# Kernel tuning notes

Measured on AMD Instinct MI355X. Metric: run time of the kernel, lower is better.

The kernel has to match this reference:

```python
import jax, jax.numpy as jnp
import numpy as np

D_MODEL = 256
D_INNER = 512   # expand_factor * d_model
D_STATE = 64
DT_RANK = 4     # ceil(d_model / 64)
D_CONV = 4
B = 8
L = 144


def setup_inputs() -> dict:
    key = jax.random.key(0)
    ks = jax.random.split(key, 8)
    s = lambda k, shp, sc=0.02: jax.random.normal(k, shp, jnp.float32) * sc
    x = jax.random.normal(ks[0], (B, L, D_MODEL), jnp.float32)
    lastin = jnp.zeros((B, D_INNER, D_STATE), jnp.float32)  # accepted but unused by the scan
    W_in = s(ks[1], (2 * D_INNER, D_MODEL))              # in_proj (no bias)
    conv_w = s(ks[2], (D_INNER, 1, D_CONV), 0.1)          # depthwise conv kernel [O, I/groups, K]
    conv_b = jnp.zeros((D_INNER,), jnp.float32)
    W_x = s(ks[3], (DT_RANK + 2 * D_STATE, D_INNER))      # x_proj (no bias)
    W_dt = s(ks[4], (D_INNER, DT_RANK), 0.1)
    b_dt = jnp.full((D_INNER,), -4.0, jnp.float32)        # softplus -> small dt, like mamba init
    A_log = jnp.log(jnp.tile(jnp.arange(1, D_STATE + 1, dtype=jnp.float32), (D_INNER, 1)))
    Dp = jnp.ones((D_INNER,), jnp.float32)
    W_out = s(ks[5], (D_MODEL, D_INNER))                  # out_proj (no bias)
    return dict(x=x, lastin=lastin, W_in=W_in, conv_w=conv_w, conv_b=conv_b,
                W_x=W_x, W_dt=W_dt, b_dt=b_dt, A_log=A_log, Dp=Dp, W_out=W_out)


def _forward(x, lastin, W_in, conv_w, conv_b, W_x, W_dt, b_dt, A_log, Dp, W_out):
    # in_proj and split
    xz = jnp.einsum('bld,ed->ble', x, W_in)               # [B, L, 2*d_inner]
    ix, z = jnp.split(xz, 2, axis=-1)

    # depthwise causal-ish conv1d: torch padding=2 then slice [:L] == padding (2, 1)
    ix = jnp.swapaxes(ix, 1, 2)                            # [B, d_inner, L]
    ix = jax.lax.conv_general_dilated(
        ix, conv_w, window_strides=(1,), padding=[(2, 1)],
        feature_group_count=D_INNER, dimension_numbers=('NCH', 'OIH', 'NCH'))
    ix = ix + conv_b[None, :, None]
    ix = jnp.swapaxes(ix, 1, 2)                            # [B, L, d_inner]
    ix = jax.nn.silu(ix)

    # ssm parameterization
    A = -jnp.exp(A_log)                                    # [d_inner, d_state]
    dBC = jnp.einsum('bld,ed->ble', ix, W_x)               # [B, L, dt_rank + 2*d_state]
    dt_r = dBC[..., :DT_RANK]
    Bm = dBC[..., DT_RANK:DT_RANK + D_STATE]               # [B, L, d_state]
    Cm = dBC[..., DT_RANK + D_STATE:]                      # [B, L, d_state]
    delta = jax.nn.softplus(jnp.einsum('blr,dr->bld', dt_r, W_dt) + b_dt)  # [B, L, d_inner]

    # discretization
    deltaA = jnp.exp(delta[..., None] * A)                 # [B, L, d_inner, d_state]
    BX = (delta * ix)[..., None] * Bm[:, :, None, :]       # [B, L, d_inner, d_state]

    # sequential selective scan: h_t = deltaA_t * h_{t-1} + BX_t
    def step(h, inp):
        dA_t, bx_t = inp
        h = dA_t * h + bx_t
        return h, h

    h0 = jnp.zeros((x.shape[0], D_INNER, D_STATE), x.dtype)
    _, hs = jax.lax.scan(step, h0, (jnp.moveaxis(deltaA, 1, 0), jnp.moveaxis(BX, 1, 0)))
    # hs: [L, B, d_inner, d_state]

    y = jnp.einsum('lbdn,lbn->bld', hs, jnp.moveaxis(Cm, 1, 0))  # [B, L, d_inner]
    y = y + Dp * ix

    out = jnp.einsum('bld,ed->ble', y * jax.nn.silu(z), W_out)   # [B, L, d_model]
    return out


def reference(x, lastin, W_in, conv_w, conv_b, W_x, W_dt, b_dt, A_log, Dp, W_out):
    return _forward(x, lastin, W_in, conv_w, conv_b, W_x, W_dt, b_dt, A_log, Dp, W_out)
```

## Files before the change

kernel.cpp:

```cpp
#include <hip/hip_runtime.h>

#define B_SZ 8
#define L_SEQ 144
#define NTOK 1152
#define D_MODEL 256
#define D_INNER 512
#define D_STATE 64
#define DT_RANK 4
#define NDBC 132
#define SLAB 152064
#define XZSLAB 1179648

#define BM 64
#define BN 64
#define BK 16

__device__ __forceinline__ int bc_perm(const int p) {
    return (p < DT_RANK) ? p
         : (((p - DT_RANK) & 1) ? (DT_RANK + D_STATE + ((p - DT_RANK) >> 1))
                                : (DT_RANK + ((p - DT_RANK) >> 1)));
}

template<bool A_MK, bool GN, bool CONV, bool PERM, bool A2S>
__global__ __launch_bounds__(256) void gemm_k(const float* __restrict__ A,
                                              const float* __restrict__ Bm,
                                              float* __restrict__ C,
                                              const int N, const int lda, const int ldb,
                                              const int ldc,
                                              const float* __restrict__ cw,
                                              const float* __restrict__ cb,
                                              const int kslab, const size_t sstride,
                                              const size_t a2off) {
    __shared__ float As[BK][BM + 4];
    __shared__ float Bs[BK][BN + 4];
    const int tid = threadIdx.x;
    const int m0 = blockIdx.y * BM;
    const int n0 = blockIdx.x * BN;
    const int kbeg = blockIdx.z * kslab;
    const int kend = kbeg + kslab;
    const int ty = tid >> 4, tx = tid & 15;
    const int lrow = tid >> 2, kq = (tid & 3) * 4;
    const int kk = tid >> 4, cc = (tid & 15) * 4;
    const int brow = PERM ? bc_perm(n0 + lrow) : (n0 + lrow);
    float acc[4][4] = {};
    float4 av, bv, cw4;
    float xm2 = 0.f, xm1 = 0.f, xp4 = 0.f, cbv = 0.f;

    auto loadA = [&](const int k0) {
        if (A_MK) {
            av = *(const float4*)(A + (size_t)(m0 + lrow) * lda + k0 + kq);
        } else {
            const float* row = A + (size_t)(k0 + kk) * lda + m0 + cc;
            av = *(const float4*)row;
            if (A2S) {
                const float4 a2 = *(const float4*)(row + a2off);
                av.x += a2.x; av.y += a2.y; av.z += a2.z; av.w += a2.w;
            }
            if (CONV) {
                const int t = (m0 + cc) % L_SEQ;
                xm2 = (t > 0) ? row[-2] : 0.f;
                xm1 = (t > 0) ? row[-1] : 0.f;
                xp4 = (t < L_SEQ - 4) ? row[4] : 0.f;
                if (A2S) {
                    if (t > 0) { xm2 += row[a2off - 2]; xm1 += row[a2off - 1]; }
                    if (t < L_SEQ - 4) xp4 += row[a2off + 4];
                }
                cw4 = *(const float4*)(cw + (k0 + kk) * 4);
                cbv = cb[k0 + kk];
            }
        }
        if (!GN || (n0 + lrow) < N)
            bv = *(const float4*)(Bm + (size_t)brow * ldb + k0 + kq);
    };

    auto storeLDS = [&]() {
        if (A_MK) {
            As[kq + 0][lrow] = av.x; As[kq + 1][lrow] = av.y;
            As[kq + 2][lrow] = av.z; As[kq + 3][lrow] = av.w;
        } else if (CONV) {
            const float in7[7] = {xm2, xm1, av.x, av.y, av.z, av.w, xp4};
            float4 o;
            float* op = &o.x;
#pragma unroll
            for (int j = 0; j < 4; ++j) {
                float s = cbv;
                s = fmaf(cw4.x, in7[j + 0], s);
                s = fmaf(cw4.y, in7[j + 1], s);
                s = fmaf(cw4.z, in7[j + 2], s);
                s = fmaf(cw4.w, in7[j + 3], s);
                op[j] = s * __builtin_amdgcn_rcpf(1.f + __expf(-s));
            }
            *(float4*)&As[kk][cc] = o;
        } else {
            *(float4*)&As[kk][cc] = av;
        }
        Bs[kq + 0][lrow] = bv.x; Bs[kq + 1][lrow] = bv.y;
        Bs[kq + 2][lrow] = bv.z; Bs[kq + 3][lrow] = bv.w;
    };

    bv = make_float4(0.f, 0.f, 0.f, 0.f);
    loadA(kbeg);
    for (int k0 = kbeg; k0 < kend; k0 += BK) {
        __syncthreads();
        storeLDS();
        __syncthreads();
        if (k0 + BK < kend) loadA(k0 + BK);
#pragma unroll
        for (int k = 0; k < BK; ++k) {
            const float4 a4 = *(const float4*)&As[k][ty * 4];
            const float4 b4 = *(const float4*)&Bs[k][tx * 4];
            const float a_[4] = {a4.x, a4.y, a4.z, a4.w};
            const float b_[4] = {b4.x, b4.y, b4.z, b4.w};
#pragma unroll
            for (int i = 0; i < 4; ++i)
#pragma unroll
                for (int j = 0; j < 4; ++j)
                    acc[i][j] = fmaf(a_[i], b_[j], acc[i][j]);
        }
    }
    C += (size_t)blockIdx.z * sstride;
#pragma unroll
    for (int i = 0; i < 4; ++i) {
        const int gm = m0 + ty * 4 + i;
        const int gn = n0 + tx * 4;
        if (!GN || gn < N)
            *(float4*)(C + (size_t)gm * ldc + gn) =
                make_float4(acc[i][0], acc[i][1], acc[i][2], acc[i][3]);
    }
}

__global__ __launch_bounds__(256) void reduce8_k(const float4* __restrict__ in,
                                                 float4* __restrict__ out,
                                                 const int n4, const int s4) {
    const int i = blockIdx.x * 256 + threadIdx.x;
    if (i >= n4) return;
    float4 a = in[i];
#pragma unroll
    for (int s = 1; s < 8; ++s) {
        const float4 b = in[i + s * s4];
        a.x += b.x; a.y += b.y; a.z += b.z; a.w += b.w;
    }
    out[i] = a;
}

__device__ __forceinline__ float bcast(const float v, const int i) {
    return __int_as_float(__builtin_amdgcn_readlane(__float_as_int(v), i));
}

template<int CNT>
__device__ __forceinline__ void scan_chunk(const float* __restrict__ dBC,
                                           const float* __restrict__ xz,
                                           float* __restrict__ gT,
                                           float (*__restrict__ Pw)[65],
                                           const int d, const int base, const int t0,
                                           const float An2, const float4 wdt,
                                           const float bdt, const float dpv,
                                           const float4 cw4, const float cbv,
                                           const int lane, float& h) {
    float delta_r = 0.f, dix_r = 0.f, dpix_r = 0.f, sz_r = 0.f;
    if (lane < CNT) {
        const int t = t0 + lane;
        const int tok = base + t;
        const float* row = xz + (size_t)d * NTOK + tok;
        float s0 = cbv;
        if (t >= 2) s0 = fmaf(cw4.x, row[-2] + row[XZSLAB - 2], s0);
        if (t >= 1) s0 = fmaf(cw4.y, row[-1] + row[XZSLAB - 1], s0);
        s0 = fmaf(cw4.z, row[0] + row[XZSLAB], s0);
        if (t < L_SEQ - 1) s0 = fmaf(cw4.w, row[1] + row[XZSLAB + 1], s0);
        const float ixv = s0 * __builtin_amdgcn_rcpf(1.f + __expf(-s0));

        const float4 dt4 = *(const float4*)(dBC + (size_t)tok * NDBC);
        float s = fmaf(dt4.x, wdt.x, bdt);
        s = fmaf(dt4.y, wdt.y, s);
        s = fmaf(dt4.z, wdt.z, s);
        s = fmaf(dt4.w, wdt.w, s);
        const float delta = fmaxf(s, 0.f) + __logf(1.f + __expf(-fabsf(s)));
        const float* zp = xz + (size_t)(D_INNER + d) * NTOK + tok;
        const float zv = zp[0] + zp[XZSLAB];
        delta_r = delta;
        dix_r   = delta * ixv;
        dpix_r  = dpv * ixv;
        sz_r    = zv * __builtin_amdgcn_rcpf(1.f + __expf(-zv));
    }
#pragma unroll
    for (int i = 0; i < CNT; ++i) {
        const float2 bc = *(const float2*)(dBC + (size_t)(base + t0 + i) * NDBC
                                           + DT_RANK + 2 * lane);
        const float dlt = bcast(delta_r, i);
        const float dxv = bcast(dix_r, i);
        const float dA = __builtin_amdgcn_exp2f(dlt * An2);
        h = fmaf(dA, h, dxv * bc.x);
        Pw[i][lane] = h * bc.y;
    }
    const int tl = lane & 31, hf = lane >> 5;
    float s2 = 0.f;
    if (tl < CNT) {
#pragma unroll
        for (int j = 0; j < 32; ++j) s2 += Pw[tl][hf * 32 + j];
    }
    s2 += __shfl_xor(s2, 32, 64);
    if (hf == 0 && tl < CNT) {
        gT[(size_t)d * NTOK + base + t0 + tl] = (s2 + dpix_r) * sz_r;
    }
}

__global__ __launch_bounds__(256) void scan_k(const float* __restrict__ dBC,
                                              const float* __restrict__ xz,
                                              const float* __restrict__ W_dt,
                                              const float* __restrict__ b_dt,
                                              const float* __restrict__ A_log,
                                              const float* __restrict__ Dp,
                                              const float* __restrict__ conv_w,
                                              const float* __restrict__ conv_b,
                                              float* __restrict__ gT) {
    __shared__ float P[4][32][65];
    const int w = threadIdx.x >> 6, lane = threadIdx.x & 63;
    const int b = blockIdx.x >> 7, dg = blockIdx.x & 127;
    const int d = (dg << 2) | w;
    const int base = b * L_SEQ;
    const float An2 = -__expf(A_log[(d << 6) + lane]) * 1.44269504088896f;
    const float4 wdt = *(const float4*)(W_dt + (d << 2));
    const float bdt = b_dt[d], dpv = Dp[d];
    const float4 cw4 = *(const float4*)(conv_w + (d << 2));
    const float cbv = conv_b[d];
    float h = 0.f;
    scan_chunk<32>(dBC, xz, gT, P[w], d, base, 0,   An2, wdt, bdt, dpv, cw4, cbv, lane, h);
    scan_chunk<32>(dBC, xz, gT, P[w], d, base, 32,  An2, wdt, bdt, dpv, cw4, cbv, lane, h);
    scan_chunk<32>(dBC, xz, gT, P[w], d, base, 64,  An2, wdt, bdt, dpv, cw4, cbv, lane, h);
    scan_chunk<32>(dBC, xz, gT, P[w], d, base, 96,  An2, wdt, bdt, dpv, cw4, cbv, lane, h);
    scan_chunk<16>(dBC, xz, gT, P[w], d, base, 128, An2, wdt, bdt, dpv, cw4, cbv, lane, h);
}

extern "C" void kernel_launch(void* const* d_in, const int* in_sizes, int n_in,
                              void* d_out, int out_size, void* d_ws, size_t ws_size,
                              hipStream_t stream) {
    const float* x      = (const float*)d_in[0];
    const float* W_in   = (const float*)d_in[2];
    const float* conv_w = (const float*)d_in[3];
    const float* conv_b = (const float*)d_in[4];
    const float* W_x    = (const float*)d_in[5];
    const float* W_dt   = (const float*)d_in[6];
    const float* b_dt   = (const float*)d_in[7];
    const float* A_log  = (const float*)d_in[8];
    const float* Dp     = (const float*)d_in[9];
    const float* W_out  = (const float*)d_in[10];
    float* out = (float*)d_out;

    float* ws  = (float*)d_ws;
    float* xz  = ws;
    float* dBC = xz + 2 * XZSLAB;
    float* gT  = dBC + 152064;
    float* sl3 = gT + 589824;
    float* sl6 = ws;

    gemm_k<true, false, false, false, false><<<dim3(18, 16, 2), 256, 0, stream>>>(
        W_in, x, xz, NTOK, D_MODEL, D_MODEL, NTOK, nullptr, nullptr, 128,
        (size_t)XZSLAB, 0);
    gemm_k<false, true, true, true, true><<<dim3(3, 18, 8), 256, 0, stream>>>(
        xz, W_x, sl3, NDBC, NTOK, D_INNER, NDBC, conv_w, conv_b, 64, (size_t)SLAB,
        (size_t)XZSLAB);
    reduce8_k<<<dim3(149), 256, 0, stream>>>((const float4*)sl3, (float4*)dBC,
                                             NTOK * NDBC / 4, NTOK * NDBC / 4);
    scan_k<<<dim3(B_SZ * 128), 256, 0, stream>>>(dBC, xz, W_dt, b_dt, A_log, Dp,
                                                 conv_w, conv_b, gT);
    gemm_k<false, false, false, false, false><<<dim3(4, 18, 8), 256, 0, stream>>>(
        gT, W_out, sl6, D_MODEL, NTOK, D_INNER, D_MODEL, nullptr, nullptr, 64,
        (size_t)NTOK * D_MODEL, 0);
    reduce8_k<<<dim3(288), 256, 0, stream>>>((const float4*)sl6, (float4*)out,
                                             NTOK * D_MODEL / 4, NTOK * D_MODEL / 4);
}
```

Baseline: 139.4 us.

## Use split-bf16 MFMA for in_proj and out_proj GEMMs

Replaces the FP32 SIMT in_proj and out_proj GEMMs with MFMA kernels that split each fp32 operand into bf16 hi and lo parts and accumulate three products, approximating fp32 accuracy. The in_proj GEMM no longer uses a split-K slab pair, so the conv/x_proj and scan stages read a single xz buffer instead of summing two slabs. The scan now writes its gated output as token-major hi/lo bf16 arrays for direct MFMA consumption. The cost is extra conversion arithmetic, small precision loss from dropping the lo*lo term, and scattered 16-bit stores from the scan.

```diff
diff --git a/kernel.cpp b/kernel.cpp
--- a/kernel.cpp
+++ b/kernel.cpp
@@ -9,11 +9,139 @@
 #define DT_RANK 4
 #define NDBC 132
 #define SLAB 152064
-#define XZSLAB 1179648
 
 #define BM 64
 #define BN 64
 #define BK 16
+
+typedef __attribute__((ext_vector_type(8))) short bf16x8;
+typedef __attribute__((ext_vector_type(4))) float f32x4;
+
+__device__ __forceinline__ void cvt8(const float4& f0, const float4& f1,
+                                     int4& hi, int4& lo) {
+    const float f[8] = {f0.x, f0.y, f0.z, f0.w, f1.x, f1.y, f1.z, f1.w};
+    unsigned h[8], l[8];
+#pragma unroll
+    for (int e = 0; e < 8; ++e) {
+        const unsigned u = __float_as_uint(f[e]);
+        const unsigned t = u + 0x7FFFu + ((u >> 16) & 1u);
+        h[e] = t >> 16;
+        l[e] = __float_as_uint(f[e] - __uint_as_float(t & 0xFFFF0000u)) >> 16;
+    }
+    hi = make_int4((int)(h[0] | (h[1] << 16)), (int)(h[2] | (h[3] << 16)),
+                   (int)(h[4] | (h[5] << 16)), (int)(h[6] | (h[7] << 16)));
+    lo = make_int4((int)(l[0] | (l[1] << 16)), (int)(l[2] | (l[3] << 16)),
+                   (int)(l[4] | (l[5] << 16)), (int)(l[6] | (l[7] << 16)));
+}
+
+#define LW 40
+__global__ __launch_bounds__(256) void gemm1_mfma(const float* __restrict__ W_in,
+                                                  const float* __restrict__ x,
+                                                  float* __restrict__ xz) {
+    __shared__ unsigned short Ah[64][LW], Al[64][LW], Bh[64][LW], Bl[64][LW];
+    const int tid = threadIdx.x;
+    const int m0 = blockIdx.y * 64, n0 = blockIdx.x * 64;
+    const int r = tid >> 2, kq = (tid & 3) * 8;
+    const int w = tid >> 6, lane = tid & 63;
+    const int wm = (w & 1) * 32, wn = (w >> 1) * 32;
+    const int fr = lane & 15, fk = (lane >> 4) * 8;
+    f32x4 acc[2][2] = {};
+    float4 a0, a1, b0, b1;
+
+    auto loadG = [&](const int k0) {
+        const float* ap = W_in + (size_t)(m0 + r) * D_MODEL + k0 + kq;
+        const float* bp = x    + (size_t)(n0 + r) * D_MODEL + k0 + kq;
+        a0 = *(const float4*)ap; a1 = *(const float4*)(ap + 4);
+        b0 = *(const float4*)bp; b1 = *(const float4*)(bp + 4);
+    };
+
+    loadG(0);
+    for (int k0 = 0; k0 < D_MODEL; k0 += 32) {
+        int4 hi, lo;
+        __syncthreads();
+        cvt8(a0, a1, hi, lo);
+        *(int4*)&Ah[r][kq] = hi; *(int4*)&Al[r][kq] = lo;
+        cvt8(b0, b1, hi, lo);
+        *(int4*)&Bh[r][kq] = hi; *(int4*)&Bl[r][kq] = lo;
+        __syncthreads();
+        if (k0 + 32 < D_MODEL) loadG(k0 + 32);
+        bf16x8 ah[2], al[2], bh[2], bl[2];
+#pragma unroll
+        for (int i = 0; i < 2; ++i) {
+            ah[i] = *(const bf16x8*)&Ah[wm + 16 * i + fr][fk];
+            al[i] = *(const bf16x8*)&Al[wm + 16 * i + fr][fk];
+            bh[i] = *(const bf16x8*)&Bh[wn + 16 * i + fr][fk];
+            bl[i] = *(const bf16x8*)&Bl[wn + 16 * i + fr][fk];
+        }
+#pragma unroll
+        for (int i = 0; i < 2; ++i)
+#pragma unroll
+            for (int j = 0; j < 2; ++j) {
+                acc[i][j] = __builtin_amdgcn_mfma_f32_16x16x32_bf16(ah[i], bh[j], acc[i][j], 0, 0, 0);
+                acc[i][j] = __builtin_amdgcn_mfma_f32_16x16x32_bf16(ah[i], bl[j], acc[i][j], 0, 0, 0);
+                acc[i][j] = __builtin_amdgcn_mfma_f32_16x16x32_bf16(al[i], bh[j], acc[i][j], 0, 0, 0);
+            }
+    }
+    const int orow = (lane >> 4) * 4;
+#pragma unroll
+    for (int i = 0; i < 2; ++i)
+#pragma unroll
+        for (int j = 0; j < 2; ++j)
+#pragma unroll
+            for (int q = 0; q < 4; ++q)
+                xz[(size_t)(m0 + wm + 16 * i + orow + q) * NTOK
+                   + n0 + wn + 16 * j + fr] = acc[i][j][q];
+}
+
+__global__ __launch_bounds__(256) void gemm3_mfma(const unsigned short* __restrict__ ghi,
+                                                  const unsigned short* __restrict__ glo,
+                                                  const float* __restrict__ W_out,
+                                                  float* __restrict__ slab) {
+    const int tid = threadIdx.x;
+    const int n0 = blockIdx.x * 64, m0 = blockIdx.y * 64;
+    const int kbeg = blockIdx.z * 64;
+    const int w = tid >> 6, lane = tid & 63;
+    const int wm = (w & 1) * 32, wn = (w >> 1) * 32;
+    const int fr = lane & 15, fk = (lane >> 4) * 8;
+    f32x4 acc[2][2] = {};
+    slab += (size_t)blockIdx.z * (NTOK * D_MODEL);
+#pragma unroll
+    for (int ks = 0; ks < 2; ++ks) {
+        const int k0 = kbeg + ks * 32;
+        bf16x8 ah[2], al[2], bh[2], bl[2];
+#pragma unroll
+        for (int i = 0; i < 2; ++i) {
+            const size_t ao = (size_t)(m0 + wm + 16 * i + fr) * D_INNER + k0 + fk;
+            ah[i] = *(const bf16x8*)(ghi + ao);
+            al[i] = *(const bf16x8*)(glo + ao);
+        }
+#pragma unroll
+        for (int j = 0; j < 2; ++j) {
+            const float* bp = W_out + (size_t)(n0 + wn + 16 * j + fr) * D_INNER + k0 + fk;
+            int4 hi, lo;
+            cvt8(*(const float4*)bp, *(const float4*)(bp + 4), hi, lo);
+            bh[j] = *(bf16x8*)&hi;
+            bl[j] = *(bf16x8*)&lo;
+        }
+#pragma unroll
+        for (int i = 0; i < 2; ++i)
+#pragma unroll
+            for (int j = 0; j < 2; ++j) {
+                acc[i][j] = __builtin_amdgcn_mfma_f32_16x16x32_bf16(ah[i], bh[j], acc[i][j], 0, 0, 0);
+                acc[i][j] = __builtin_amdgcn_mfma_f32_16x16x32_bf16(ah[i], bl[j], acc[i][j], 0, 0, 0);
+                acc[i][j] = __builtin_amdgcn_mfma_f32_16x16x32_bf16(al[i], bh[j], acc[i][j], 0, 0, 0);
+            }
+    }
+    const int orow = (lane >> 4) * 4;
+#pragma unroll
+    for (int i = 0; i < 2; ++i)
+#pragma unroll
+        for (int j = 0; j < 2; ++j)
+#pragma unroll
+            for (int q = 0; q < 4; ++q)
+                slab[(size_t)(m0 + wm + 16 * i + orow + q) * D_MODEL
+                     + n0 + wn + 16 * j + fr] = acc[i][j][q];
+}
 
 __device__ __forceinline__ int bc_perm(const int p) {
     return (p < DT_RANK) ? p
@@ -21,7 +149,7 @@
                                 : (DT_RANK + ((p - DT_RANK) >> 1)));
 }
 
-template<bool A_MK, bool GN, bool CONV, bool PERM, bool A2S>
+template<bool A_MK, bool GN, bool CONV, bool PERM>
 __global__ __launch_bounds__(256) void gemm_k(const float* __restrict__ A,
                                               const float* __restrict__ Bm,
                                               float* __restrict__ C,
@@ -29,8 +157,7 @@
                                               const int ldc,
                                               const float* __restrict__ cw,
                                               const float* __restrict__ cb,
-                                              const int kslab, const size_t sstride,
-                                              const size_t a2off) {
+                                              const int kslab, const size_t sstride) {
     __shared__ float As[BK][BM + 4];
     __shared__ float Bs[BK][BN + 4];
     const int tid = threadIdx.x;
@@ -52,19 +179,11 @@
         } else {
             const float* row = A + (size_t)(k0 + kk) * lda + m0 + cc;
             av = *(const float4*)row;
-            if (A2S) {
-                const float4 a2 = *(const float4*)(row + a2off);
-                av.x += a2.x; av.y += a2.y; av.z += a2.z; av.w += a2.w;
-            }
             if (CONV) {
                 const int t = (m0 + cc) % L_SEQ;
                 xm2 = (t > 0) ? row[-2] : 0.f;
                 xm1 = (t > 0) ? row[-1] : 0.f;
                 xp4 = (t < L_SEQ - 4) ? row[4] : 0.f;
-                if (A2S) {
-                    if (t > 0) { xm2 += row[a2off - 2]; xm1 += row[a2off - 1]; }
-                    if (t < L_SEQ - 4) xp4 += row[a2off + 4];
-                }
                 cw4 = *(const float4*)(cw + (k0 + kk) * 4);
                 cbv = cb[k0 + kk];
             }
@@ -150,7 +269,8 @@
 template<int CNT>
 __device__ __forceinline__ void scan_chunk(const float* __restrict__ dBC,
                                            const float* __restrict__ xz,
-                                           float* __restrict__ gT,
+                                           unsigned short* __restrict__ ghi,
+                                           unsigned short* __restrict__ glo,
                                            float (*__restrict__ Pw)[65],
                                            const int d, const int base, const int t0,
                                            const float An2, const float4 wdt,
@@ -163,10 +283,10 @@
         const int tok = base + t;
         const float* row = xz + (size_t)d * NTOK + tok;
         float s0 = cbv;
-        if (t >= 2) s0 = fmaf(cw4.x, row[-2] + row[XZSLAB - 2], s0);
-        if (t >= 1) s0 = fmaf(cw4.y, row[-1] + row[XZSLAB - 1], s0);
-        s0 = fmaf(cw4.z, row[0] + row[XZSLAB], s0);
-        if (t < L_SEQ - 1) s0 = fmaf(cw4.w, row[1] + row[XZSLAB + 1], s0);
+        if (t >= 2) s0 = fmaf(cw4.x, row[-2], s0);
+        if (t >= 1) s0 = fmaf(cw4.y, row[-1], s0);
+        s0 = fmaf(cw4.z, row[0], s0);
+        if (t < L_SEQ - 1) s0 = fmaf(cw4.w, row[1], s0);
         const float ixv = s0 * __builtin_amdgcn_rcpf(1.f + __expf(-s0));
 
         const float4 dt4 = *(const float4*)(dBC + (size_t)tok * NDBC);
@@ -175,8 +295,7 @@
         s = fmaf(dt4.z, wdt.z, s);
         s = fmaf(dt4.w, wdt.w, s);
         const float delta = fmaxf(s, 0.f) + __logf(1.f + __expf(-fabsf(s)));
-        const float* zp = xz + (size_t)(D_INNER + d) * NTOK + tok;
-        const float zv = zp[0] + zp[XZSLAB];
+        const float zv = xz[(size_t)(D_INNER + d) * NTOK + tok];
         delta_r = delta;
         dix_r   = delta * ixv;
         dpix_r  = dpv * ixv;
@@ -200,7 +319,13 @@
     }
     s2 += __shfl_xor(s2, 32, 64);
     if (hf == 0 && tl < CNT) {
-        gT[(size_t)d * NTOK + base + t0 + tl] = (s2 + dpix_r) * sz_r;
+        const float g = (s2 + dpix_r) * sz_r;
+        const unsigned u = __float_as_uint(g);
+        const unsigned t = u + 0x7FFFu + ((u >> 16) & 1u);
+        const size_t o = (size_t)(base + t0 + tl) * D_INNER + d;
+        ghi[o] = (unsigned short)(t >> 16);
+        glo[o] = (unsigned short)(__float_as_uint(
+                     g - __uint_as_float(t & 0xFFFF0000u)) >> 16);
     }
 }
 
@@ -212,7 +337,8 @@
                                               const float* __restrict__ Dp,
                                               const float* __restrict__ conv_w,
                                               const float* __restrict__ conv_b,
-                                              float* __restrict__ gT) {
+                                              unsigned short* __restrict__ ghi,
+                                              unsigned short* __restrict__ glo) {
     __shared__ float P[4][32][65];
     const int w = threadIdx.x >> 6, lane = threadIdx.x & 63;
     const int b = blockIdx.x >> 7, dg = blockIdx.x & 127;
@@ -224,11 +350,11 @@
     const float4 cw4 = *(const float4*)(conv_w + (d << 2));
     const float cbv = conv_b[d];
     float h = 0.f;
-    scan_chunk<32>(dBC, xz, gT, P[w], d, base, 0,   An2, wdt, bdt, dpv, cw4, cbv, lane, h);
-    scan_chunk<32>(dBC, xz, gT, P[w], d, base, 32,  An2, wdt, bdt, dpv, cw4, cbv, lane, h);
-    scan_chunk<32>(dBC, xz, gT, P[w], d, base, 64,  An2, wdt, bdt, dpv, cw4, cbv, lane, h);
-    scan_chunk<32>(dBC, xz, gT, P[w], d, base, 96,  An2, wdt, bdt, dpv, cw4, cbv, lane, h);
-    scan_chunk<16>(dBC, xz, gT, P[w], d, base, 128, An2, wdt, bdt, dpv, cw4, cbv, lane, h);
+    scan_chunk<32>(dBC, xz, ghi, glo, P[w], d, base, 0,   An2, wdt, bdt, dpv, cw4, cbv, lane, h);
+    scan_chunk<32>(dBC, xz, ghi, glo, P[w], d, base, 32,  An2, wdt, bdt, dpv, cw4, cbv, lane, h);
+    scan_chunk<32>(dBC, xz, ghi, glo, P[w], d, base, 64,  An2, wdt, bdt, dpv, cw4, cbv, lane, h);
+    scan_chunk<32>(dBC, xz, ghi, glo, P[w], d, base, 96,  An2, wdt, bdt, dpv, cw4, cbv, lane, h);
+    scan_chunk<16>(dBC, xz, ghi, glo, P[w], d, base, 128, An2, wdt, bdt, dpv, cw4, cbv, lane, h);
 }
 
 extern "C" void kernel_launch(void* const* d_in, const int* in_sizes, int n_in,
@@ -248,24 +374,20 @@
 
     float* ws  = (float*)d_ws;
     float* xz  = ws;
-    float* dBC = xz + 2 * XZSLAB;
-    float* gT  = dBC + 152064;
-    float* sl3 = gT + 589824;
-    float* sl6 = ws;
-
-    gemm_k<true, false, false, false, false><<<dim3(18, 16, 2), 256, 0, stream>>>(
-        W_in, x, xz, NTOK, D_MODEL, D_MODEL, NTOK, nullptr, nullptr, 128,
-        (size_t)XZSLAB, 0);
-    gemm_k<false, true, true, true, true><<<dim3(3, 18, 8), 256, 0, stream>>>(
-        xz, W_x, sl3, NDBC, NTOK, D_INNER, NDBC, conv_w, conv_b, 64, (size_t)SLAB,
-        (size_t)XZSLAB);
+    float* dBC = xz + 1179648;
+    float* sl3 = dBC + 152064;
+    unsigned short* ghi = (unsigned short*)(sl3 + 8 * SLAB);
+    unsigned short* glo = ghi + NTOK * D_INNER;
+    float* sl6 = (float*)(glo + NTOK * D_INNER);
+
+    gemm1_mfma<<<dim3(18, 16), 256, 0, stream>>>(W_in, x, xz);
+    gemm_k<false, true, true, true><<<dim3(3, 18, 8), 256, 0, stream>>>(
+        xz, W_x, sl3, NDBC, NTOK, D_INNER, NDBC, conv_w, conv_b, 64, (size_t)SLAB);
     reduce8_k<<<dim3(149), 256, 0, stream>>>((const float4*)sl3, (float4*)dBC,
                                              NTOK * NDBC / 4, NTOK * NDBC / 4);
     scan_k<<<dim3(B_SZ * 128), 256, 0, stream>>>(dBC, xz, W_dt, b_dt, A_log, Dp,
-                                                 conv_w, conv_b, gT);
-    gemm_k<false, false, false, false, false><<<dim3(4, 18, 8), 256, 0, stream>>>(
-        gT, W_out, sl6, D_MODEL, NTOK, D_INNER, D_MODEL, nullptr, nullptr, 64,
-        (size_t)NTOK * D_MODEL, 0);
+                                                 conv_w, conv_b, ghi, glo);
+    gemm3_mfma<<<dim3(4, 18, 8), 256, 0, stream>>>(ghi, glo, W_out, sl6);
     reduce8_k<<<dim3(288), 256, 0, stream>>>((const float4*)sl6, (float4*)out,
                                              NTOK * D_MODEL / 4, NTOK * D_MODEL / 4);
 }
```

Result: faster. 136.4 us (-2.2%).
